# Kernel tuning notes

Hardware: AMD Instinct MI355X
Metric: run time of the kernel (lower is better)

The kernel has to match this reference:

```python
import jax, jax.numpy as jnp
import numpy as np

D = 1024          # d_model == d_memory
N_LAYERS = 4      # memory MLP depth
EPS = 1e-5        # LayerNorm epsilon (no scale/bias in original)


def _layernorm(x):
    mu = jnp.mean(x, axis=-1, keepdims=True)
    var = jnp.var(x, axis=-1, keepdims=True)
    return (x - mu) * jax.lax.rsqrt(var + EPS)


def setup_inputs() -> dict:
    key = jax.random.key(0)
    ks = jax.random.split(key, 8)
    x = jax.random.normal(ks[0], (4, 4096, D), dtype=jnp.float32)
    # projection params (normal std 0.02, zero bias, matching flax init)
    wq = jax.random.normal(ks[1], (D, D), dtype=jnp.float32) * 0.02
    bq = jnp.zeros((D,), dtype=jnp.float32)
    w_out = jax.random.normal(ks[2], (D, D), dtype=jnp.float32) * 0.02
    b_out = jnp.zeros((D,), dtype=jnp.float32)
    # memory MLP: 4 layers, all D x D (d_in = d_hidden = d_out = D), stacked
    mlp_w = jax.random.normal(ks[3], (N_LAYERS, D, D), dtype=jnp.float32) * 0.02
    mlp_b = jnp.zeros((N_LAYERS, D), dtype=jnp.float32)
    return {"x": x, "wq": wq, "bq": bq, "mlp_w": mlp_w, "mlp_b": mlp_b,
            "w_out": w_out, "b_out": b_out}


def reference(x, wq, bq, mlp_w, mlp_b, w_out, b_out):
    # retrieve(): y = W_out( M*(LN(W_Q(x))) + straight-through(q_norm) )
    q = jnp.einsum("bsd,de->bse", x, wq) + bq
    q_norm = _layernorm(q)
    # memory MLP weights get stop_gradient in the original
    mw = jax.lax.stop_gradient(mlp_w)
    mb = jax.lax.stop_gradient(mlp_b)
    h = q_norm
    for i in range(N_LAYERS):
        h = jnp.einsum("bsd,de->bse", h, mw[i]) + mb[i]
        if i < N_LAYERS - 1:
            h = jax.nn.silu(h)
    # straight-through trick: zero in the forward, passes grad to q_norm
    out = h + (q_norm - jax.lax.stop_gradient(q_norm))
    return jnp.einsum("bsd,de->bse", out, w_out) + b_out
```

## Files before the change

kernel.cpp:

```cpp
#include <hip/hip_runtime.h>
#include <hip/hip_bf16.h>
#include <math.h>

#define D_MODEL 1024
#define DD (1024 * 1024)

typedef unsigned short ushort_t;
using short8 = __attribute__((ext_vector_type(8))) short;
using f32x4  = __attribute__((ext_vector_type(4))) float;

#define ACT_NONE 0
#define ACT_SILU 1

__device__ __forceinline__ float bf2f(ushort_t u) {
    return __uint_as_float(((unsigned int)u) << 16);
}
__device__ __forceinline__ ushort_t f2bf(float f) {
    unsigned int x = __float_as_uint(f);
    x += 0x7fffu + ((x >> 16) & 1u);
    return (ushort_t)(x >> 16);
}

#define GL2LDS(gp, lp)                                                         \
    __builtin_amdgcn_global_load_lds(                                          \
        (const __attribute__((address_space(1))) void*)(gp),                   \
        (__attribute__((address_space(3))) void*)(lp), 16, 0, 0)

template <int ACT, int OUTF32, int BIASF>
__global__ __launch_bounds__(512, 2) void gemm256(
    const ushort_t* __restrict__ A,
    const ushort_t* __restrict__ Bt,
    const float* __restrict__ bias,
    void* __restrict__ Cv, int M)
{
    constexpr int K = 1024, N = 1024;
    constexpr int NU = K / 32;
    __shared__ ushort_t lds[4 * 16384];

    const int tid  = threadIdx.x;
    const int lane = tid & 63;
    const int wave = tid >> 6;
    const int quad = lane >> 4;
    const int lr   = lane & 15;
    const int wm   = wave >> 2;
    const int wn   = wave & 3;
    const int bm   = blockIdx.x;
    const int bn   = blockIdx.y;

    const ushort_t* Ab = A  + (size_t)bm * 256 * K;
    const ushort_t* Bb = Bt + (size_t)bn * 256 * K;

    const int sg    = (tid & 3) ^ ((tid >> 3) & 3);
    const size_t s0 = (size_t)(tid >> 2) * K + (size_t)sg * 8;
    const size_t s1 = s0 + (size_t)128 * K;
    const int d0 = tid * 8;
    const int d1 = tid * 8 + 4096;

    const int chk  = quad ^ ((lr >> 1) & 3);
    const int aoff = (wm * 128 + lr) * 32 + chk * 8;
    const int boff = (wn * 64  + lr) * 32 + chk * 8;

    f32x4 acc[8][4];
#pragma unroll
    for (int i = 0; i < 8; i++)
#pragma unroll
        for (int j = 0; j < 4; j++) acc[i][j] = (f32x4){0.f, 0.f, 0.f, 0.f};

#define SA256(su) do { const int b_ = ((su) & 3) * 16384;                      \
        GL2LDS(Ab + s0 + (su) * 32, lds + b_ + d0);                            \
        GL2LDS(Ab + s1 + (su) * 32, lds + b_ + d1); } while (0)
#define SB256(su) do { const int b_ = ((su) & 3) * 16384 + 8192;               \
        GL2LDS(Bb + s0 + (su) * 32, lds + b_ + d0);                           \
        GL2LDS(Bb + s1 + (su) * 32, lds + b_ + d1); } while (0)

    SA256(0); SB256(0);
    SA256(1); SB256(1);
    SA256(2); SB256(2);
    asm volatile("s_waitcnt vmcnt(4)" ::: "memory");
    __builtin_amdgcn_s_barrier();

    short8 afr[4], bfr[4];
#pragma unroll
    for (int u = 0; u < NU; u += 2) {
        {
            const ushort_t* Ax = lds + (u & 3) * 16384;
            const ushort_t* Bx = Ax + 8192;
#pragma unroll
            for (int t = 0; t < 4; t++)
                bfr[t] = *(const short8*)(Bx + boff + t * 512);
#pragma unroll
            for (int t = 0; t < 4; t++)
                afr[t] = *(const short8*)(Ax + aoff + t * 512);
            if (u + 3 < NU) SA256(u + 3);
            __builtin_amdgcn_s_barrier();
            asm volatile("s_waitcnt lgkmcnt(0)" ::: "memory");
            __builtin_amdgcn_sched_barrier(0);
            __builtin_amdgcn_s_setprio(1);
#pragma unroll
            for (int mt = 0; mt < 4; mt++)
#pragma unroll
                for (int nt = 0; nt < 4; nt++)
                    acc[mt][nt] = __builtin_amdgcn_mfma_f32_16x16x32_bf16(
                        afr[mt], bfr[nt], acc[mt][nt], 0, 0, 0);
            __builtin_amdgcn_s_setprio(0);
            __builtin_amdgcn_s_barrier();
#pragma unroll
            for (int t = 0; t < 4; t++)
                afr[t] = *(const short8*)(Ax + aoff + (4 + t) * 512);
            if (u + 3 < NU) SB256(u + 3);
            __builtin_amdgcn_s_barrier();
            asm volatile("s_waitcnt lgkmcnt(0)" ::: "memory");
            __builtin_amdgcn_sched_barrier(0);
            __builtin_amdgcn_s_setprio(1);
#pragma unroll
            for (int mt = 0; mt < 4; mt++)
#pragma unroll
                for (int nt = 0; nt < 4; nt++)
                    acc[mt + 4][nt] = __builtin_amdgcn_mfma_f32_16x16x32_bf16(
                        afr[mt], bfr[nt], acc[mt + 4][nt], 0, 0, 0);
            __builtin_amdgcn_s_setprio(0);
            __builtin_amdgcn_s_barrier();
        }
        {
            const ushort_t* Ax = lds + ((u + 1) & 3) * 16384;
            const ushort_t* Bx = Ax + 8192;
#pragma unroll
            for (int t = 0; t < 4; t++)
                bfr[t] = *(const short8*)(Bx + boff + t * 512);
#pragma unroll
            for (int t = 0; t < 4; t++)
                afr[t] = *(const short8*)(Ax + aoff + t * 512);
            if (u + 4 < NU) SA256(u + 4);
            __builtin_amdgcn_s_barrier();
            asm volatile("s_waitcnt lgkmcnt(0)" ::: "memory");
            __builtin_amdgcn_sched_barrier(0);
            __builtin_amdgcn_s_setprio(1);
#pragma unroll
            for (int mt = 0; mt < 4; mt++)
#pragma unroll
                for (int nt = 0; nt < 4; nt++)
                    acc[mt][nt] = __builtin_amdgcn_mfma_f32_16x16x32_bf16(
                        afr[mt], bfr[nt], acc[mt][nt], 0, 0, 0);
            __builtin_amdgcn_s_setprio(0);
            __builtin_amdgcn_s_barrier();
#pragma unroll
            for (int t = 0; t < 4; t++)
                afr[t] = *(const short8*)(Ax + aoff + (4 + t) * 512);
            if (u + 4 < NU) SB256(u + 4);
            __builtin_amdgcn_s_barrier();
            asm volatile("s_waitcnt lgkmcnt(0)" ::: "memory");
            __builtin_amdgcn_sched_barrier(0);
            __builtin_amdgcn_s_setprio(1);
#pragma unroll
            for (int mt = 0; mt < 4; mt++)
#pragma unroll
                for (int nt = 0; nt < 4; nt++)
                    acc[mt + 4][nt] = __builtin_amdgcn_mfma_f32_16x16x32_bf16(
                        afr[mt], bfr[nt], acc[mt + 4][nt], 0, 0, 0);
            __builtin_amdgcn_s_setprio(0);
            if (u + 4 >= NU)
                asm volatile("s_waitcnt vmcnt(0)" ::: "memory");
            else
                asm volatile("s_waitcnt vmcnt(4)" ::: "memory");
            __builtin_amdgcn_s_barrier();
        }
    }
#undef SA256
#undef SB256

    float bv[4];
#pragma unroll
    for (int nt = 0; nt < 4; nt++)
        bv[nt] = BIASF ? bias[bn * 256 + wn * 64 + nt * 16 + lr] : 0.f;

#pragma unroll
    for (int mt = 0; mt < 8; mt++) {
#pragma unroll
        for (int nt = 0; nt < 4; nt++) {
            const int col = bn * 256 + wn * 64 + nt * 16 + lr;
#pragma unroll
            for (int r = 0; r < 4; r++) {
                const int row = bm * 256 + wm * 128 + mt * 16 + quad * 4 + r;
                float v = acc[mt][nt][r] + bv[nt];
                if (ACT == ACT_SILU) v = v / (1.f + __expf(-v));
                if (OUTF32)
                    ((float*)Cv)[(size_t)row * N + col] = v;
                else
                    ((ushort_t*)Cv)[(size_t)row * N + col] = f2bf(v);
            }
        }
    }
}

template <int ACT, int OUTF32, int BIASF>
__global__ __launch_bounds__(256) void gemm_bf16(
    const ushort_t* __restrict__ A,
    const ushort_t* __restrict__ Bt,
    const float* __restrict__ bias,
    void* __restrict__ Cv, int M)
{
    constexpr int K = 1024, N = 1024;
    __shared__ ushort_t As[128 * 32];
    __shared__ ushort_t Bs[128 * 32];

    const int tid  = threadIdx.x;
    const int lane = tid & 63;
    const int wave = tid >> 6;
    const int quad = lane >> 4;
    const int lr   = lane & 15;
    const int bm   = blockIdx.x;
    const int bn   = blockIdx.y;
    const int wm   = (wave >> 1) * 64;
    const int wn   = (wave & 1) * 64;

    f32x4 acc[4][4];
#pragma unroll
    for (int i = 0; i < 4; i++)
#pragma unroll
        for (int j = 0; j < 4; j++) acc[i][j] = (f32x4){0.f, 0.f, 0.f, 0.f};

    int ci0 = tid, ci1 = tid + 256;
    int am0 = ci0 >> 2, akc0 = (ci0 & 3) ^ ((am0 >> 1) & 3);
    int am1 = ci1 >> 2, akc1 = (ci1 & 3) ^ ((am1 >> 1) & 3);
    const ushort_t* Ab = A + (size_t)(bm * 128) * K;
    const ushort_t* Bb = Bt + (size_t)(bn * 128) * K;

    for (int k0 = 0; k0 < K; k0 += 32) {
        GL2LDS(Ab + (size_t)am0 * K + k0 + akc0 * 8, As + ci0 * 8);
        GL2LDS(Ab + (size_t)am1 * K + k0 + akc1 * 8, As + ci1 * 8);
        GL2LDS(Bb + (size_t)am0 * K + k0 + akc0 * 8, Bs + ci0 * 8);
        GL2LDS(Bb + (size_t)am1 * K + k0 + akc1 * 8, Bs + ci1 * 8);
        __syncthreads();

        short8 af[4], bfr[4];
#pragma unroll
        for (int t = 0; t < 4; t++) {
            int m = wm + t * 16 + lr;
            af[t] = *(const short8*)(As + m * 32 + ((quad ^ ((m >> 1) & 3)) * 8));
            int n = wn + t * 16 + lr;
            bfr[t] = *(const short8*)(Bs + n * 32 + ((quad ^ ((n >> 1) & 3)) * 8));
        }
#pragma unroll
        for (int mt = 0; mt < 4; mt++)
#pragma unroll
            for (int nt = 0; nt < 4; nt++)
                acc[mt][nt] = __builtin_amdgcn_mfma_f32_16x16x32_bf16(
                    af[mt], bfr[nt], acc[mt][nt], 0, 0, 0);
        __syncthreads();
    }

    float bv[4];
#pragma unroll
    for (int nt = 0; nt < 4; nt++)
        bv[nt] = BIASF ? bias[bn * 128 + wn + nt * 16 + lr] : 0.f;

#pragma unroll
    for (int mt = 0; mt < 4; mt++) {
#pragma unroll
        for (int nt = 0; nt < 4; nt++) {
            const int col = bn * 128 + wn + nt * 16 + lr;
#pragma unroll
            for (int r = 0; r < 4; r++) {
                const int row = bm * 128 + wm + mt * 16 + quad * 4 + r;
                float v = acc[mt][nt][r] + bv[nt];
                if (ACT == ACT_SILU) v = v / (1.f + __expf(-v));
                if (OUTF32)
                    ((float*)Cv)[(size_t)row * N + col] = v;
                else
                    ((ushort_t*)Cv)[(size_t)row * N + col] = f2bf(v);
            }
        }
    }
}

__global__ __launch_bounds__(256) void layernorm_bf16(ushort_t* __restrict__ X)
{
    const int row = blockIdx.x;
    const int tid = threadIdx.x;
    ushort_t* x = X + (size_t)row * D_MODEL + tid * 4;

    uint2 u = *(uint2*)x;
    float a = bf2f(u.x & 0xffff), b = bf2f(u.x >> 16);
    float c = bf2f(u.y & 0xffff), d = bf2f(u.y >> 16);
    float s = a + b + c + d;
    float ss = a * a + b * b + c * c + d * d;

#pragma unroll
    for (int off = 32; off > 0; off >>= 1) {
        s += __shfl_down(s, off);
        ss += __shfl_down(ss, off);
    }
    __shared__ float sbuf[4], ssbuf[4];
    const int wave = tid >> 6;
    if ((tid & 63) == 0) { sbuf[wave] = s; ssbuf[wave] = ss; }
    __syncthreads();
    const float S = sbuf[0] + sbuf[1] + sbuf[2] + sbuf[3];
    const float SS = ssbuf[0] + ssbuf[1] + ssbuf[2] + ssbuf[3];
    const float mu = S * (1.f / D_MODEL);
    const float var = SS * (1.f / D_MODEL) - mu * mu;
    const float r = rsqrtf(var + 1e-5f);

    a = (a - mu) * r; b = (b - mu) * r; c = (c - mu) * r; d = (d - mu) * r;
    u.x = (unsigned)f2bf(a) | ((unsigned)f2bf(b) << 16);
    u.y = (unsigned)f2bf(c) | ((unsigned)f2bf(d) << 16);
    *(uint2*)x = u;
}

__global__ __launch_bounds__(256) void prep_all(
    const float* __restrict__ wq, const float* __restrict__ mlp_w,
    const float* __restrict__ w_out, const float* __restrict__ x,
    const float* __restrict__ b3, const float* __restrict__ bout,
    ushort_t* __restrict__ wt, ushort_t* __restrict__ Q,
    float* __restrict__ bf, int nxblk)
{
    const int blk = blockIdx.x;
    const int tid = threadIdx.x;

    if (blk < 6144) {
        const int z = blk >> 10;
        const int t = blk & 1023;
        const int k0 = (t >> 5) * 32;
        const int n0 = (t & 31) * 32;
        const int r = tid >> 5;
        const int c = tid & 31;

        if (z == 5) {
            const float* src = mlp_w + (size_t)3 * DD;
            ushort_t* dst = wt + (size_t)5 * DD;
#pragma unroll
            for (int i = 0; i < 4; i++) {
                size_t idx = (size_t)(k0 + r + 8 * i) * D_MODEL + n0 + c;
                dst[idx] = f2bf(src[idx]);
            }
            return;
        }
        const float* src = (z == 0) ? wq : (z < 4) ? (mlp_w + (size_t)(z - 1) * DD) : w_out;
        ushort_t* dst = wt + (size_t)z * DD;
        __shared__ float tile[32][33];
#pragma unroll
        for (int i = 0; i < 4; i++)
            tile[r + 8 * i][c] = src[(size_t)(k0 + r + 8 * i) * D_MODEL + n0 + c];
        __syncthreads();
#pragma unroll
        for (int i = 0; i < 4; i++)
            dst[(size_t)(n0 + r + 8 * i) * D_MODEL + k0 + c] = f2bf(tile[c][r + 8 * i]);
        return;
    }
    if (blk < 6144 + nxblk) {
        int i = (blk - 6144) * 256 + tid;
        const float4* p = (const float4*)(x + (size_t)i * 8);
        float4 v0 = p[0], v1 = p[1];
        union { ushort_t u[8]; uint4 v; } pk;
        pk.u[0] = f2bf(v0.x); pk.u[1] = f2bf(v0.y);
        pk.u[2] = f2bf(v0.z); pk.u[3] = f2bf(v0.w);
        pk.u[4] = f2bf(v1.x); pk.u[5] = f2bf(v1.y);
        pk.u[6] = f2bf(v1.z); pk.u[7] = f2bf(v1.w);
        *(uint4*)(Q + (size_t)i * 8) = pk.v;
        return;
    }
    {
        const int b = blk - 6144 - nxblk;
        const int n = b * 32 + (tid & 31);
        const int kg = tid >> 5;
        float s = 0.f;
        for (int k = kg * 128; k < (kg + 1) * 128; k++)
            s = fmaf(b3[k], w_out[(size_t)k * D_MODEL + n], s);
        __shared__ float red[8][32];
        red[kg][tid & 31] = s;
        __syncthreads();
        if (kg == 0) {
            float t = 0.f;
#pragma unroll
            for (int j = 0; j < 8; j++) t += red[j][tid & 31];
            bf[n] = t + bout[n];
        }
    }
}

extern "C" void kernel_launch(void* const* d_in, const int* in_sizes, int n_in,
                              void* d_out, int out_size, void* d_ws, size_t ws_size,
                              hipStream_t stream)
{
    const float* x     = (const float*)d_in[0];
    const float* wq    = (const float*)d_in[1];
    const float* bq    = (const float*)d_in[2];
    const float* mlp_w = (const float*)d_in[3];
    const float* mlp_b = (const float*)d_in[4];
    const float* w_out = (const float*)d_in[5];
    const float* b_out = (const float*)d_in[6];

    const int D = D_MODEL;
    const int M = in_sizes[0] / D;

    ushort_t* wt  = (ushort_t*)d_ws;
    ushort_t* w3b = wt + (size_t)5 * DD;
    ushort_t* wtF = wt + (size_t)6 * DD;
    ushort_t* Q   = wt + (size_t)7 * DD;
    float*    bf  = (float*)(Q + (size_t)M * D);
    ushort_t* P   = (ushort_t*)d_out;

    const int nxblk = M * D / 2048;
    prep_all<<<6144 + nxblk + 32, 256, 0, stream>>>(
        wq, mlp_w, w_out, x, mlp_b + 3 * D, b_out, wt, Q, bf, nxblk);
    gemm_bf16<ACT_NONE, 0, 0><<<dim3(8, 8), 256, 0, stream>>>(
        wt + (size_t)4 * DD, w3b, nullptr, wtF, 1024);

    if ((M & 255) == 0) {
        dim3 grid(M / 256, D / 256);
        gemm256<ACT_NONE, 0, 1><<<grid, 512, 0, stream>>>(Q, wt + (size_t)0 * DD, bq, P, M);
        layernorm_bf16<<<M, 256, 0, stream>>>(P);
        gemm256<ACT_SILU, 0, 1><<<grid, 512, 0, stream>>>(P, wt + (size_t)1 * DD, mlp_b + 0 * D, Q, M);
        gemm256<ACT_SILU, 0, 1><<<grid, 512, 0, stream>>>(Q, wt + (size_t)2 * DD, mlp_b + 1 * D, P, M);
        gemm256<ACT_SILU, 0, 1><<<grid, 512, 0, stream>>>(P, wt + (size_t)3 * DD, mlp_b + 2 * D, Q, M);
        gemm256<ACT_NONE, 1, 1><<<grid, 512, 0, stream>>>(Q, wtF, bf, d_out, M);
    } else {
        dim3 grid(M / 128, D / 128);
        gemm_bf16<ACT_NONE, 0, 1><<<grid, 256, 0, stream>>>(Q, wt + (size_t)0 * DD, bq, P, M);
        layernorm_bf16<<<M, 256, 0, stream>>>(P);
        gemm_bf16<ACT_SILU, 0, 1><<<grid, 256, 0, stream>>>(P, wt + (size_t)1 * DD, mlp_b + 0 * D, Q, M);
        gemm_bf16<ACT_SILU, 0, 1><<<grid, 256, 0, stream>>>(Q, wt + (size_t)2 * DD, mlp_b + 1 * D, P, M);
        gemm_bf16<ACT_SILU, 0, 1><<<grid, 256, 0, stream>>>(P, wt + (size_t)3 * DD, mlp_b + 2 * D, Q, M);
        gemm_bf16<ACT_NONE, 1, 1><<<grid, 256, 0, stream>>>(Q, wtF, bf, d_out, M);
    }
}
```

Measured before the change: 356.0 us.

## Software-pipeline LDS fragment reads across K-steps in bf16 GEMM main loop

Replaces the two-stage unrolled GEMM loop with a single-stage loop. A fragments are split into even and odd register sets, and the next step's A and B fragment reads from LDS are issued during the current step's MFMAs. Full lgkmcnt(0) waits become partial lgkmcnt(4) waits, and some barriers are removed, so LDS latency overlaps with matrix math. This costs extra registers. The reworked vmcnt accounting in the tail iterations, where no new global loads are issued, may leave LDS data races.

```diff
diff --git a/kernel.cpp b/kernel.cpp
--- a/kernel.cpp
+++ b/kernel.cpp
@@ -60,113 +60,87 @@
     const int aoff = (wm * 128 + lr) * 32 + chk * 8;
     const int boff = (wn * 64  + lr) * 32 + chk * 8;
 
+    short8 bfr[4], afrE[4], afrO[4];
     f32x4 acc[8][4];
 #pragma unroll
     for (int i = 0; i < 8; i++)
 #pragma unroll
         for (int j = 0; j < 4; j++) acc[i][j] = (f32x4){0.f, 0.f, 0.f, 0.f};
 
-#define SA256(su) do { const int b_ = ((su) & 3) * 16384;                      \
-        GL2LDS(Ab + s0 + (su) * 32, lds + b_ + d0);                            \
-        GL2LDS(Ab + s1 + (su) * 32, lds + b_ + d1); } while (0)
-#define SB256(su) do { const int b_ = ((su) & 3) * 16384 + 8192;               \
-        GL2LDS(Bb + s0 + (su) * 32, lds + b_ + d0);                           \
-        GL2LDS(Bb + s1 + (su) * 32, lds + b_ + d1); } while (0)
-
-    SA256(0); SB256(0);
-    SA256(1); SB256(1);
-    SA256(2); SB256(2);
-    asm volatile("s_waitcnt vmcnt(4)" ::: "memory");
+#define SA(v) do { const int b_ = ((v) & 3) * 16384;                           \
+        GL2LDS(Ab + s0 + (v) * 32, lds + b_ + d0);                             \
+        GL2LDS(Ab + s1 + (v) * 32, lds + b_ + d1); } while (0)
+#define SB(v) do { const int b_ = ((v) & 3) * 16384 + 8192;                    \
+        GL2LDS(Bb + s0 + (v) * 32, lds + b_ + d0);                             \
+        GL2LDS(Bb + s1 + (v) * 32, lds + b_ + d1); } while (0)
+#define RAE(v) do { const ushort_t* p_ = lds + ((v) & 3) * 16384 + aoff;       \
+        afrE[0] = *(const short8*)(p_);                                        \
+        afrE[1] = *(const short8*)(p_ + 512);                                  \
+        afrE[2] = *(const short8*)(p_ + 1024);                                 \
+        afrE[3] = *(const short8*)(p_ + 1536); } while (0)
+#define RAO(v) do { const ushort_t* p_ = lds + ((v) & 3) * 16384 + aoff + 2048;\
+        afrO[0] = *(const short8*)(p_);                                        \
+        afrO[1] = *(const short8*)(p_ + 512);                                  \
+        afrO[2] = *(const short8*)(p_ + 1024);                                 \
+        afrO[3] = *(const short8*)(p_ + 1536); } while (0)
+#define RB(v) do { const ushort_t* p_ = lds + ((v) & 3) * 16384 + 8192 + boff; \
+        bfr[0] = *(const short8*)(p_);                                         \
+        bfr[1] = *(const short8*)(p_ + 512);                                   \
+        bfr[2] = *(const short8*)(p_ + 1024);                                  \
+        bfr[3] = *(const short8*)(p_ + 1536); } while (0)
+
+    SA(0); SB(0);
+    SA(1); SB(1);
+    SA(2); SB(2);
+    asm volatile("s_waitcnt vmcnt(8)" ::: "memory");
     __builtin_amdgcn_s_barrier();
-
-    short8 afr[4], bfr[4];
-#pragma unroll
-    for (int u = 0; u < NU; u += 2) {
-        {
-            const ushort_t* Ax = lds + (u & 3) * 16384;
-            const ushort_t* Bx = Ax + 8192;
-#pragma unroll
-            for (int t = 0; t < 4; t++)
-                bfr[t] = *(const short8*)(Bx + boff + t * 512);
-#pragma unroll
-            for (int t = 0; t < 4; t++)
-                afr[t] = *(const short8*)(Ax + aoff + t * 512);
-            if (u + 3 < NU) SA256(u + 3);
-            __builtin_amdgcn_s_barrier();
+    RAE(0);
+    RB(0);
+    __builtin_amdgcn_sched_barrier(0);
+
+#pragma unroll
+    for (int u = 0; u < NU; ++u) {
+        RAO(u);
+        asm volatile("s_waitcnt vmcnt(4)" ::: "memory");
+        __builtin_amdgcn_s_barrier();
+        if (u + 3 < NU) SA(u + 3);
+        asm volatile("s_waitcnt lgkmcnt(4)" ::: "memory");
+        __builtin_amdgcn_sched_barrier(0);
+        __builtin_amdgcn_s_setprio(1);
+#pragma unroll
+        for (int mt = 0; mt < 4; mt++)
+#pragma unroll
+            for (int nt = 0; nt < 4; nt++)
+                acc[mt][nt] = __builtin_amdgcn_mfma_f32_16x16x32_bf16(
+                    afrE[mt], bfr[nt], acc[mt][nt], 0, 0, 0);
+        __builtin_amdgcn_s_setprio(0);
+        if (u + 1 < NU) RAE(u + 1);
+        asm volatile("s_waitcnt vmcnt(4)" ::: "memory");
+        __builtin_amdgcn_s_barrier();
+        if (u + 3 < NU) SB(u + 3);
+        if (u + 1 < NU)
+            asm volatile("s_waitcnt lgkmcnt(4)" ::: "memory");
+        else
             asm volatile("s_waitcnt lgkmcnt(0)" ::: "memory");
+        __builtin_amdgcn_sched_barrier(0);
+        __builtin_amdgcn_s_setprio(1);
+#pragma unroll
+        for (int mt = 0; mt < 4; mt++)
+#pragma unroll
+            for (int nt = 0; nt < 4; nt++)
+                acc[mt + 4][nt] = __builtin_amdgcn_mfma_f32_16x16x32_bf16(
+                    afrO[mt], bfr[nt], acc[mt + 4][nt], 0, 0, 0);
+        __builtin_amdgcn_s_setprio(0);
+        if (u + 1 < NU) {
+            RB(u + 1);
             __builtin_amdgcn_sched_barrier(0);
-            __builtin_amdgcn_s_setprio(1);
-#pragma unroll
-            for (int mt = 0; mt < 4; mt++)
-#pragma unroll
-                for (int nt = 0; nt < 4; nt++)
-                    acc[mt][nt] = __builtin_amdgcn_mfma_f32_16x16x32_bf16(
-                        afr[mt], bfr[nt], acc[mt][nt], 0, 0, 0);
-            __builtin_amdgcn_s_setprio(0);
-            __builtin_amdgcn_s_barrier();
-#pragma unroll
-            for (int t = 0; t < 4; t++)
-                afr[t] = *(const short8*)(Ax + aoff + (4 + t) * 512);
-            if (u + 3 < NU) SB256(u + 3);
-            __builtin_amdgcn_s_barrier();
-            asm volatile("s_waitcnt lgkmcnt(0)" ::: "memory");
-            __builtin_amdgcn_sched_barrier(0);
-            __builtin_amdgcn_s_setprio(1);
-#pragma unroll
-            for (int mt = 0; mt < 4; mt++)
-#pragma unroll
-                for (int nt = 0; nt < 4; nt++)
-                    acc[mt + 4][nt] = __builtin_amdgcn_mfma_f32_16x16x32_bf16(
-                        afr[mt], bfr[nt], acc[mt + 4][nt], 0, 0, 0);
-            __builtin_amdgcn_s_setprio(0);
-            __builtin_amdgcn_s_barrier();
-        }
-        {
-            const ushort_t* Ax = lds + ((u + 1) & 3) * 16384;
-            const ushort_t* Bx = Ax + 8192;
-#pragma unroll
-            for (int t = 0; t < 4; t++)
-                bfr[t] = *(const short8*)(Bx + boff + t * 512);
-#pragma unroll
-            for (int t = 0; t < 4; t++)
-                afr[t] = *(const short8*)(Ax + aoff + t * 512);
-            if (u + 4 < NU) SA256(u + 4);
-            __builtin_amdgcn_s_barrier();
-            asm volatile("s_waitcnt lgkmcnt(0)" ::: "memory");
-            __builtin_amdgcn_sched_barrier(0);
-            __builtin_amdgcn_s_setprio(1);
-#pragma unroll
-            for (int mt = 0; mt < 4; mt++)
-#pragma unroll
-                for (int nt = 0; nt < 4; nt++)
-                    acc[mt][nt] = __builtin_amdgcn_mfma_f32_16x16x32_bf16(
-                        afr[mt], bfr[nt], acc[mt][nt], 0, 0, 0);
-            __builtin_amdgcn_s_setprio(0);
-            __builtin_amdgcn_s_barrier();
-#pragma unroll
-            for (int t = 0; t < 4; t++)
-                afr[t] = *(const short8*)(Ax + aoff + (4 + t) * 512);
-            if (u + 4 < NU) SB256(u + 4);
-            __builtin_amdgcn_s_barrier();
-            asm volatile("s_waitcnt lgkmcnt(0)" ::: "memory");
-            __builtin_amdgcn_sched_barrier(0);
-            __builtin_amdgcn_s_setprio(1);
-#pragma unroll
-            for (int mt = 0; mt < 4; mt++)
-#pragma unroll
-                for (int nt = 0; nt < 4; nt++)
-                    acc[mt + 4][nt] = __builtin_amdgcn_mfma_f32_16x16x32_bf16(
-                        afr[mt], bfr[nt], acc[mt + 4][nt], 0, 0, 0);
-            __builtin_amdgcn_s_setprio(0);
-            if (u + 4 >= NU)
-                asm volatile("s_waitcnt vmcnt(0)" ::: "memory");
-            else
-                asm volatile("s_waitcnt vmcnt(4)" ::: "memory");
-            __builtin_amdgcn_s_barrier();
-        }
-    }
-#undef SA256
-#undef SB256
+        }
+    }
+#undef SA
+#undef SB
+#undef RAE
+#undef RAO
+#undef RB
 
     float bv[4];
 #pragma unroll
```

Result: no change. 354.5 us (-0.4%).
